# Performance work log

Hardware: AMD Instinct MI355X
Metric: run time of the kernel (lower is better)

## Reference

```python
import jax, jax.numpy as jnp
import numpy as np

N = 200000          # num nodes (num_rus)
E = 12800000        # num edges (avg degree 64)
IN_C, HID, OUT = 1, 16, 4


def setup_inputs() -> dict:
    key = jax.random.key(0)
    ks = jax.random.split(key, 6)
    x = jax.random.normal(ks[0], (N, IN_C), dtype=jnp.float32)
    edges = jax.random.randint(ks[1], (2, E), 0, N, dtype=jnp.int64)
    W1 = jax.random.normal(ks[2], (IN_C, HID), dtype=jnp.float32) / np.sqrt(IN_C)
    b1 = jnp.zeros((HID,), dtype=jnp.float32)
    W2 = jax.random.normal(ks[3], (HID, HID), dtype=jnp.float32) / np.sqrt(HID)
    b2 = jnp.zeros((HID,), dtype=jnp.float32)
    Wl = jax.random.normal(ks[4], (HID, OUT), dtype=jnp.float32) / np.sqrt(HID)
    bl = jnp.zeros((OUT,), dtype=jnp.float32)
    return {"x": x, "edges": edges, "W1": W1, "b1": b1, "W2": W2, "b2": b2, "Wl": Wl, "bl": bl}


def _gcn_norm(edges):
    # PyG GCNConv default: add self-loops, symmetric normalization.
    loops = jnp.arange(N, dtype=edges.dtype)
    src = jnp.concatenate([edges[0], loops])   # [E+N]
    dst = jnp.concatenate([edges[1], loops])
    deg = jax.ops.segment_sum(jnp.ones_like(dst, dtype=jnp.float32), dst, num_segments=N)
    dinv = jnp.where(deg > 0, jax.lax.rsqrt(deg), 0.0)
    norm = dinv[src] * dinv[dst]               # [E+N]
    return src, dst, norm


def _gcn_conv(h, W, b, src, dst, norm):
    m = h @ W                                  # [N, out] transform first (cheap, small C)
    msgs = m[src] * norm[:, None]              # gather + normalize, [E+N, out]
    agg = jax.ops.segment_sum(msgs, dst, num_segments=N)
    return agg + b


def reference(x, edges, W1, b1, W2, b2, Wl, bl):
    src, dst, norm = _gcn_norm(edges)
    h = jax.nn.relu(_gcn_conv(x, W1, b1, src, dst, norm))
    h = jax.nn.relu(_gcn_conv(h, W2, b2, src, dst, norm))
    return h @ Wl + bl                         # [N, 4]
```

## Files before the change

kernel.cpp:

```cpp
#include <hip/hip_runtime.h>

#define HID 16
#define OUTC 4
#define G 64
#define SBSH 8
#define SBN 256
#define CAP 17408
#define PHSH 15
#define SUBK 8
#define KB (SBN * SUBK)
#define CHUNKS 256
#define PBLK 512
#define NPB_MAX 1024

__device__ __forceinline__ float relu(float v) { return v > 0.f ? v : 0.f; }

__global__ void k_cnt(const int* __restrict__ dst, int* __restrict__ cnt, int E, int nsb) {
    __shared__ int lc[NPB_MAX];
    for (int i = threadIdx.x; i < nsb; i += PBLK) lc[i] = 0;
    __syncthreads();
    int c = blockIdx.x;
    int chunk = (E + CHUNKS - 1) / CHUNKS;
    int lo = c * chunk, hi = lo + chunk < E ? lo + chunk : E;
    for (int i = lo + threadIdx.x; i < hi; i += PBLK)
        atomicAdd(lc + (dst[i] >> SBSH), 1);
    __syncthreads();
    for (int b = threadIdx.x; b < nsb; b += PBLK)
        cnt[b * CHUNKS + c] = lc[b];
}

__global__ void k_scanA(int* __restrict__ a, int* __restrict__ bsum, int L) {
    __shared__ int s[1024];
    int i = blockIdx.x * 1024 + threadIdx.x;
    int v = (i < L) ? a[i] : 0;
    s[threadIdx.x] = v; __syncthreads();
    for (int off = 1; off < 1024; off <<= 1) {
        int t = (threadIdx.x >= (unsigned)off) ? s[threadIdx.x - off] : 0;
        __syncthreads();
        s[threadIdx.x] += t;
        __syncthreads();
    }
    if (i < L) a[i] = s[threadIdx.x] - v;
    if (threadIdx.x == 1023) bsum[blockIdx.x] = s[1023];
}

__global__ void k_scanB(int* __restrict__ bsum, int SB) {
    __shared__ int s[1024];
    int carry = 0;
    for (int base = 0; base < SB; base += 1024) {
        int idx = base + threadIdx.x;
        int v = (idx < SB) ? bsum[idx] : 0;
        s[threadIdx.x] = v; __syncthreads();
        for (int off = 1; off < 1024; off <<= 1) {
            int t = (threadIdx.x >= (unsigned)off) ? s[threadIdx.x - off] : 0;
            __syncthreads();
            s[threadIdx.x] += t;
            __syncthreads();
        }
        if (idx < SB) bsum[idx] = carry + s[threadIdx.x] - v;
        carry += s[1023];
        __syncthreads();
    }
}

__global__ void k_scanC(int* __restrict__ a, const int* __restrict__ bsum,
                        int* __restrict__ bOff, int L, int nsb, int E) {
    int i = blockIdx.x * 1024 + threadIdx.x;
    if (i < L) {
        int v = a[i] + bsum[blockIdx.x];
        a[i] = v;
        if ((i & (CHUNKS - 1)) == 0) bOff[i / CHUNKS] = v;
    }
    if (i == 0) bOff[nsb] = E;
}

__global__ void k_part(const int* __restrict__ src, const int* __restrict__ dst,
                       const int* __restrict__ cnt, unsigned int* __restrict__ rec,
                       int E, int nsb) {
    __shared__ int cur[NPB_MAX];
    int c = blockIdx.x;
    for (int b = threadIdx.x; b < nsb; b += PBLK) cur[b] = cnt[b * CHUNKS + c];
    __syncthreads();
    int chunk = (E + CHUNKS - 1) / CHUNKS;
    int lo = c * chunk, hi = lo + chunk < E ? lo + chunk : E;
    for (int i = lo + threadIdx.x; i < hi; i += PBLK) {
        int d = dst[i], s = src[i];
        int p = atomicAdd(cur + (d >> SBSH), 1);
        rec[p] = (unsigned int)s | ((unsigned int)(d & (SBN - 1)) << 18);
    }
}

__global__ void __launch_bounds__(256) k_sort(const int* __restrict__ bOff,
                                              unsigned int* __restrict__ rec,
                                              float* __restrict__ dinv,
                                              int* __restrict__ rowp,
                                              int N, int nsb, int E) {
    __shared__ unsigned int raw[CAP];
    __shared__ int hist[KB], cur[KB];
    __shared__ int s[256];
    int b = blockIdx.x;
    int beg = bOff[b], end = bOff[b + 1];
    int size = end - beg; if (size > CAP) size = CAP;
    for (int i = threadIdx.x; i < size; i += 256) raw[i] = rec[beg + i];
    for (int k = threadIdx.x; k < KB; k += 256) hist[k] = 0;
    __syncthreads();
    for (int i = threadIdx.x; i < size; i += 256) {
        unsigned int r = raw[i];
        int key = (int)((r >> 18) << 3) | (int)((r & 0x3FFFF) >> PHSH);
        atomicAdd(hist + key, 1);
    }
    __syncthreads();
    int t = threadIdx.x;
    int psum = 0;
#pragma unroll
    for (int j = 0; j < SUBK; ++j) psum += hist[t * SUBK + j];
    s[t] = psum; __syncthreads();
    for (int off = 1; off < 256; off <<= 1) {
        int v = (t >= off) ? s[t - off] : 0;
        __syncthreads();
        s[t] += v;
        __syncthreads();
    }
    int ex = s[t] - psum;
    {
        int n = b * SBN + t;
        bool valid = (n < N);
        int running = ex;
#pragma unroll
        for (int j = 0; j < SUBK; ++j) {
            cur[t * SUBK + j] = running;
            if (valid) rowp[(size_t)n * SUBK + j] = beg + running;
            running += hist[t * SUBK + j];
        }
        if (valid) dinv[n] = rsqrtf((float)psum + 1.0f);
    }
    __syncthreads();
    for (int i = t; i < size; i += 256) {
        unsigned int r = raw[i];
        int key = (int)((r >> 18) << 3) | (int)((r & 0x3FFFF) >> PHSH);
        int p = atomicAdd(cur + key, 1);
        rec[beg + p] = r & 0x3FFFF;
    }
}

__global__ void k_m1(const float* __restrict__ x, const float* __restrict__ W1,
                     const float* __restrict__ dinv, float* __restrict__ m, int N) {
    int t = blockIdx.x * blockDim.x + threadIdx.x;
    if (t < N * HID) {
        int n = t >> 4, c = t & 15;
        m[t] = x[n] * W1[c] * dinv[n];
    }
}

__global__ void k_m2(float4* __restrict__ h4, const float* __restrict__ W2,
                     const float* __restrict__ dinv, int N) {
    __shared__ float hs[64][HID + 1];
    __shared__ float w[HID * HID];
    if (threadIdx.x < HID * HID) w[threadIdx.x] = W2[threadIdx.x];
    int idx = blockIdx.x * 256 + threadIdx.x;
    int n = idx >> 2, q = idx & 3;
    int ln = threadIdx.x >> 2;
    if (n < N) {
        float4 v = h4[idx];
        hs[ln][q * 4 + 0] = v.x; hs[ln][q * 4 + 1] = v.y;
        hs[ln][q * 4 + 2] = v.z; hs[ln][q * 4 + 3] = v.w;
    }
    __syncthreads();
    if (n < N) {
        float dn = dinv[n];
        float4 acc = make_float4(0.f, 0.f, 0.f, 0.f);
        const float* hr = hs[ln];
#pragma unroll
        for (int ci = 0; ci < HID; ++ci) {
            float hv = hr[ci];
            const float* wr = w + ci * HID + q * 4;
            acc.x += hv * wr[0]; acc.y += hv * wr[1];
            acc.z += hv * wr[2]; acc.w += hv * wr[3];
        }
        acc.x *= dn; acc.y *= dn; acc.z *= dn; acc.w *= dn;
        h4[idx] = acc;
    }
}

template <int MODE>
__global__ void __launch_bounds__(256) k_aggp(const int* __restrict__ rowp,
                                              const unsigned int* __restrict__ adj,
                                              const float* __restrict__ dinv,
                                              const float4* __restrict__ mS4,
                                              float4* __restrict__ gagg4,
                                              const float4* __restrict__ b4,
                                              const float* __restrict__ Wl,
                                              const float* __restrict__ bl,
                                              float* __restrict__ out,
                                              int N, int p) {
    __shared__ float hs[G][HID + 1];
    __shared__ float wl[HID * OUTC];
    __shared__ float blv[OUTC];
    if (MODE == 2) {
        if (threadIdx.x < HID * OUTC) wl[threadIdx.x] = Wl[threadIdx.x];
        if (threadIdx.x < OUTC) blv[threadIdx.x] = bl[threadIdx.x];
    }
    int dl = threadIdx.x >> 2, q = threadIdx.x & 3;
    int n = blockIdx.x * G + dl;
    if (n < N) {
        int i = rowp[(size_t)n * SUBK + p];
        int end = rowp[(size_t)n * SUBK + p + 1];
        float4 acc = (p == 0) ? mS4[n * 4 + q] : gagg4[n * 4 + q];
        for (; i + 4 <= end; i += 4) {
            int s0 = adj[i] * 4 + q, s1 = adj[i + 1] * 4 + q;
            int s2 = adj[i + 2] * 4 + q, s3 = adj[i + 3] * 4 + q;
            float4 v0 = mS4[s0], v1 = mS4[s1], v2 = mS4[s2], v3 = mS4[s3];
            acc.x += v0.x + v1.x + v2.x + v3.x;
            acc.y += v0.y + v1.y + v2.y + v3.y;
            acc.z += v0.z + v1.z + v2.z + v3.z;
            acc.w += v0.w + v1.w + v2.w + v3.w;
        }
        for (; i < end; ++i) {
            float4 v = mS4[adj[i] * 4 + q];
            acc.x += v.x; acc.y += v.y; acc.z += v.z; acc.w += v.w;
        }
        if (MODE == 0) {
            gagg4[n * 4 + q] = acc;
        } else {
            float dn = dinv[n];
            float4 bb = b4[q];
            float4 h;
            h.x = relu(acc.x * dn + bb.x);
            h.y = relu(acc.y * dn + bb.y);
            h.z = relu(acc.z * dn + bb.z);
            h.w = relu(acc.w * dn + bb.w);
            if (MODE == 1) {
                gagg4[n * 4 + q] = h;
            } else {
                hs[dl][q * 4 + 0] = h.x; hs[dl][q * 4 + 1] = h.y;
                hs[dl][q * 4 + 2] = h.z; hs[dl][q * 4 + 3] = h.w;
            }
        }
    }
    if (MODE == 2) {
        __syncthreads();
        if (n < N) {
            float acc = blv[q];
            const float* hr = hs[dl];
#pragma unroll
            for (int ci = 0; ci < HID; ++ci) acc += hr[ci] * wl[ci * OUTC + q];
            out[n * OUTC + q] = acc;
        }
    }
}

static inline size_t alignup(size_t v, size_t a) { return (v + a - 1) & ~(a - 1); }

extern "C" void kernel_launch(void* const* d_in, const int* in_sizes, int n_in,
                              void* d_out, int out_size, void* d_ws, size_t ws_size,
                              hipStream_t stream) {
    const float* x  = (const float*)d_in[0];
    const int* ed   = (const int*)d_in[1];
    const float* W1 = (const float*)d_in[2];
    const float* b1 = (const float*)d_in[3];
    const float* W2 = (const float*)d_in[4];
    const float* b2 = (const float*)d_in[5];
    const float* Wl = (const float*)d_in[6];
    const float* bl = (const float*)d_in[7];
    float* out      = (float*)d_out;

    int N = in_sizes[0];
    int E = in_sizes[1] / 2;
    const int* src = ed;
    const int* dst = ed + E;
    int nsb = (N + SBN - 1) / SBN;
    int nb64 = (N + G - 1) / G;
    int L = nsb * CHUNKS;
    int SB = (L + 1023) / 1024;
    int nphase = (N + (1 << PHSH) - 1) >> PHSH;

    char* w = (char*)d_ws;
    size_t o = 0;
    float* dinv       = (float*)(w + o); o = alignup(o + (size_t)N * 4, 16);
    int* rowp         = (int*)(w + o);   o = alignup(o + (size_t)N * SUBK * 4, 16);
    int* bsum         = (int*)(w + o);   o = alignup(o + (size_t)SB * 4, 16);
    int* bOff         = (int*)(w + o);   o = alignup(o + ((size_t)nsb + 1) * 4, 16);
    unsigned int* rec = (unsigned int*)(w + o); o = alignup(o + (size_t)E * 4, 16);
    float* bufA       = (float*)(w + o); o = alignup(o + (size_t)N * HID * 4, 16);
    float* bufB       = (float*)(w + o); o = alignup(o + (size_t)N * HID * 4, 16);
    int* cnt          = (int*)bufA;
    (void)ws_size;

    int blk = 256;
    int gN16 = (N * HID + blk - 1) / blk;

    k_cnt<<<CHUNKS, PBLK, 0, stream>>>(dst, cnt, E, nsb);
    k_scanA<<<SB, 1024, 0, stream>>>(cnt, bsum, L);
    k_scanB<<<1, 1024, 0, stream>>>(bsum, SB);
    k_scanC<<<SB, 1024, 0, stream>>>(cnt, bsum, bOff, L, nsb, E);
    k_part<<<CHUNKS, PBLK, 0, stream>>>(src, dst, cnt, rec, E, nsb);
    k_sort<<<nsb, 256, 0, stream>>>(bOff, rec, dinv, rowp, N, nsb, E);

    k_m1<<<gN16, blk, 0, stream>>>(x, W1, dinv, bufA, N);
    for (int p = 0; p < nphase; ++p) {
        if (p < nphase - 1)
            k_aggp<0><<<nb64, blk, 0, stream>>>(rowp, rec, dinv, (const float4*)bufA,
                                                (float4*)bufB, (const float4*)b1,
                                                nullptr, nullptr, nullptr, N, p);
        else
            k_aggp<1><<<nb64, blk, 0, stream>>>(rowp, rec, dinv, (const float4*)bufA,
                                                (float4*)bufB, (const float4*)b1,
                                                nullptr, nullptr, nullptr, N, p);
    }

    k_m2<<<nb64, blk, 0, stream>>>((float4*)bufB, W2, dinv, N);
    for (int p = 0; p < nphase; ++p) {
        if (p < nphase - 1)
            k_aggp<0><<<nb64, blk, 0, stream>>>(rowp, rec, dinv, (const float4*)bufB,
                                                (float4*)bufA, (const float4*)b2,
                                                nullptr, nullptr, nullptr, N, p);
        else
            k_aggp<2><<<nb64, blk, 0, stream>>>(rowp, rec, dinv, (const float4*)bufB,
                                                (float4*)bufA, (const float4*)b2,
                                                Wl, bl, out, N, p);
    }
}
```

Before: 622.0 us.

## Stage partition scatter in LDS and write bucket records in 64-byte runs

The partition kernel now buffers each bucket's records in shared memory and flushes them to global memory as aligned 16-element uint4 runs, instead of scattering single 4-byte writes. Per-chunk bucket counts are padded to multiples of 16, and leftover tails are filled with sentinel values that the sort kernel skips. CHUNKS is halved and CAP raised so the padded buckets still fit. The aim is coalesced global writes in exchange for extra LDS traffic, more barriers, fewer partition blocks, and padding overhead in the record array.

```diff
diff --git a/kernel.cpp b/kernel.cpp
--- a/kernel.cpp
+++ b/kernel.cpp
@@ -5,13 +5,16 @@
 #define G 64
 #define SBSH 8
 #define SBN 256
-#define CAP 17408
+#define CAP 19456
 #define PHSH 15
 #define SUBK 8
 #define KB (SBN * SUBK)
-#define CHUNKS 256
+#define CHUNKS 128
 #define PBLK 512
-#define NPB_MAX 1024
+#define NPB_MAX 800
+#define STCAP 32
+#define EPP (PBLK * 4)
+#define SENT 0xFFFFFFFFu
 
 __device__ __forceinline__ float relu(float v) { return v > 0.f ? v : 0.f; }
 
@@ -26,7 +29,7 @@
         atomicAdd(lc + (dst[i] >> SBSH), 1);
     __syncthreads();
     for (int b = threadIdx.x; b < nsb; b += PBLK)
-        cnt[b * CHUNKS + c] = lc[b];
+        cnt[b * CHUNKS + c] = (lc[b] + 15) & ~15;
 }
 
 __global__ void k_scanA(int* __restrict__ a, int* __restrict__ bsum, int L) {
@@ -61,32 +64,80 @@
         carry += s[1023];
         __syncthreads();
     }
+    if (threadIdx.x == 0) bsum[SB] = carry;
 }
 
 __global__ void k_scanC(int* __restrict__ a, const int* __restrict__ bsum,
-                        int* __restrict__ bOff, int L, int nsb, int E) {
+                        int* __restrict__ bOff, int L, int nsb, int SB) {
     int i = blockIdx.x * 1024 + threadIdx.x;
     if (i < L) {
         int v = a[i] + bsum[blockIdx.x];
         a[i] = v;
         if ((i & (CHUNKS - 1)) == 0) bOff[i / CHUNKS] = v;
     }
-    if (i == 0) bOff[nsb] = E;
-}
-
-__global__ void k_part(const int* __restrict__ src, const int* __restrict__ dst,
-                       const int* __restrict__ cnt, unsigned int* __restrict__ rec,
-                       int E, int nsb) {
-    __shared__ int cur[NPB_MAX];
+    if (blockIdx.x == 0 && threadIdx.x == 0) bOff[nsb] = bsum[SB];
+}
+
+__global__ void __launch_bounds__(PBLK) k_part(const int* __restrict__ src,
+                                               const int* __restrict__ dst,
+                                               const int* __restrict__ cnt,
+                                               unsigned int* __restrict__ rec,
+                                               int E, int nsb) {
+    __shared__ unsigned int stage[NPB_MAX][STCAP];
+    __shared__ int scnt[NPB_MAX];
+    __shared__ int gcur[NPB_MAX];
     int c = blockIdx.x;
-    for (int b = threadIdx.x; b < nsb; b += PBLK) cur[b] = cnt[b * CHUNKS + c];
+    for (int b = threadIdx.x; b < nsb; b += PBLK) {
+        scnt[b] = 0;
+        gcur[b] = cnt[b * CHUNKS + c];
+    }
     __syncthreads();
     int chunk = (E + CHUNKS - 1) / CHUNKS;
     int lo = c * chunk, hi = lo + chunk < E ? lo + chunk : E;
-    for (int i = lo + threadIdx.x; i < hi; i += PBLK) {
-        int d = dst[i], s = src[i];
-        int p = atomicAdd(cur + (d >> SBSH), 1);
-        rec[p] = (unsigned int)s | ((unsigned int)(d & (SBN - 1)) << 18);
+    for (int base = lo; base < hi; base += EPP) {
+#pragma unroll
+        for (int k = 0; k < 4; ++k) {
+            int i = base + k * PBLK + threadIdx.x;
+            if (i < hi) {
+                int d = dst[i], s = src[i];
+                int b = d >> SBSH;
+                int pos = atomicAdd(scnt + b, 1);
+                if (pos < STCAP)
+                    stage[b][pos] = (unsigned int)s | ((unsigned int)(d & (SBN - 1)) << 18);
+            }
+        }
+        __syncthreads();
+        for (int b = threadIdx.x; b < nsb; b += PBLK) {
+            int n = scnt[b];
+            int f = n & ~15;
+            if (f > 0) {
+                uint4* d4 = (uint4*)&rec[gcur[b]];
+                for (int j = 0; j < f; j += 16) {
+                    const unsigned int* sp = &stage[b][j];
+                    d4[0] = make_uint4(sp[0], sp[1], sp[2], sp[3]);
+                    d4[1] = make_uint4(sp[4], sp[5], sp[6], sp[7]);
+                    d4[2] = make_uint4(sp[8], sp[9], sp[10], sp[11]);
+                    d4[3] = make_uint4(sp[12], sp[13], sp[14], sp[15]);
+                    d4 += 4;
+                }
+                gcur[b] += f;
+                for (int j = 0; j < n - f; ++j) stage[b][j] = stage[b][f + j];
+                scnt[b] = n - f;
+            }
+        }
+        __syncthreads();
+    }
+    for (int b = threadIdx.x; b < nsb; b += PBLK) {
+        int n = scnt[b];
+        if (n > 0) {
+            unsigned int tmp[16];
+            for (int j = 0; j < 16; ++j) tmp[j] = (j < n) ? stage[b][j] : SENT;
+            uint4* d4 = (uint4*)&rec[gcur[b]];
+            d4[0] = make_uint4(tmp[0], tmp[1], tmp[2], tmp[3]);
+            d4[1] = make_uint4(tmp[4], tmp[5], tmp[6], tmp[7]);
+            d4[2] = make_uint4(tmp[8], tmp[9], tmp[10], tmp[11]);
+            d4[3] = make_uint4(tmp[12], tmp[13], tmp[14], tmp[15]);
+        }
     }
 }
 
@@ -106,6 +157,7 @@
     __syncthreads();
     for (int i = threadIdx.x; i < size; i += 256) {
         unsigned int r = raw[i];
+        if (r == SENT) continue;
         int key = (int)((r >> 18) << 3) | (int)((r & 0x3FFFF) >> PHSH);
         atomicAdd(hist + key, 1);
     }
@@ -137,6 +189,7 @@
     __syncthreads();
     for (int i = t; i < size; i += 256) {
         unsigned int r = raw[i];
+        if (r == SENT) continue;
         int key = (int)((r >> 18) << 3) | (int)((r & 0x3FFFF) >> PHSH);
         int p = atomicAdd(cur + key, 1);
         rec[beg + p] = r & 0x3FFFF;
@@ -273,16 +326,17 @@
     int L = nsb * CHUNKS;
     int SB = (L + 1023) / 1024;
     int nphase = (N + (1 << PHSH) - 1) >> PHSH;
+    size_t Epad = (size_t)E + 16 * (size_t)L;
 
     char* w = (char*)d_ws;
     size_t o = 0;
-    float* dinv       = (float*)(w + o); o = alignup(o + (size_t)N * 4, 16);
-    int* rowp         = (int*)(w + o);   o = alignup(o + (size_t)N * SUBK * 4, 16);
-    int* bsum         = (int*)(w + o);   o = alignup(o + (size_t)SB * 4, 16);
-    int* bOff         = (int*)(w + o);   o = alignup(o + ((size_t)nsb + 1) * 4, 16);
-    unsigned int* rec = (unsigned int*)(w + o); o = alignup(o + (size_t)E * 4, 16);
-    float* bufA       = (float*)(w + o); o = alignup(o + (size_t)N * HID * 4, 16);
-    float* bufB       = (float*)(w + o); o = alignup(o + (size_t)N * HID * 4, 16);
+    float* dinv       = (float*)(w + o); o = alignup(o + (size_t)N * 4, 64);
+    int* rowp         = (int*)(w + o);   o = alignup(o + (size_t)N * SUBK * 4, 64);
+    int* bsum         = (int*)(w + o);   o = alignup(o + ((size_t)SB + 1) * 4, 64);
+    int* bOff         = (int*)(w + o);   o = alignup(o + ((size_t)nsb + 1) * 4, 64);
+    unsigned int* rec = (unsigned int*)(w + o); o = alignup(o + Epad * 4, 64);
+    float* bufA       = (float*)(w + o); o = alignup(o + (size_t)N * HID * 4, 64);
+    float* bufB       = (float*)(w + o); o = alignup(o + (size_t)N * HID * 4, 64);
     int* cnt          = (int*)bufA;
     (void)ws_size;
 
@@ -292,7 +346,7 @@
     k_cnt<<<CHUNKS, PBLK, 0, stream>>>(dst, cnt, E, nsb);
     k_scanA<<<SB, 1024, 0, stream>>>(cnt, bsum, L);
     k_scanB<<<1, 1024, 0, stream>>>(bsum, SB);
-    k_scanC<<<SB, 1024, 0, stream>>>(cnt, bsum, bOff, L, nsb, E);
+    k_scanC<<<SB, 1024, 0, stream>>>(cnt, bsum, bOff, L, nsb, SB);
     k_part<<<CHUNKS, PBLK, 0, stream>>>(src, dst, cnt, rec, E, nsb);
     k_sort<<<nsb, 256, 0, stream>>>(bOff, rec, dinv, rowp, N, nsb, E);
 
```

After: 673.6 us. 8.3% more time.
